# Kernel optimization log

Measured on AMD Instinct MI355X. Metric: run time of the kernel, lower is better.

The kernel has to match this reference:

```python
import jax, jax.numpy as jnp
import numpy as np

N, C_IN, C_OUT, W_DIM, H, W = 16, 512, 512, 512, 64, 64

def setup_inputs() -> dict:
    key = jax.random.key(0)
    ks = jax.random.split(key, 6)
    return {
        "x": jax.random.normal(ks[0], (N, C_IN, H, W), dtype=jnp.float32),
        "w": jax.random.normal(ks[1], (N, W_DIM), dtype=jnp.float32),
        "noise": jax.random.normal(ks[2], (N, 1, H, W), dtype=jnp.float32),
        "affine_w": jax.random.normal(ks[3], (C_IN, W_DIM), dtype=jnp.float32) * (1.0 / np.sqrt(W_DIM)),
        "affine_b": jnp.ones((C_IN,), dtype=jnp.float32),  # bias_init=1.0
        "noise_strength": jnp.ones((), dtype=jnp.float32),
        "conv_w": jax.random.normal(ks[4], (C_OUT, C_IN, 3, 3), dtype=jnp.float32),
        "conv_b": jnp.zeros((C_OUT,), dtype=jnp.float32),
    }

def reference(x, w, noise, affine_w, affine_b, noise_strength, conv_w, conv_b):
    # affine: s = w @ affine_w.T + affine_b  (no activation)
    s = jnp.einsum('nd,cd->nc', w, affine_w) + affine_b  # [N, C_in]
    # Demodulated per-sample conv. Original builds w_n = W * s_n then demodulates;
    # since conv is linear in the weight's input-channel scale, this is equivalent to
    # scaling the input by s and the output by the demod factor d.
    w2 = jnp.sum(conv_w * conv_w, axis=(2, 3))  # [O, I]: sum over kernel taps
    d = jax.lax.rsqrt(jnp.einsum('ni,oi->no', s * s, w2) + 1e-8)  # [N, O]
    x_mod = x * s[:, :, None, None]
    y = jax.lax.conv_general_dilated(
        x_mod, conv_w, window_strides=(1, 1), padding='SAME',
        dimension_numbers=('NCHW', 'OIHW', 'NCHW'))  # [N, O, H, W]
    y = y * d[:, :, None, None] + conv_b[None, :, None, None]
    y = y + noise * noise_strength
    return jnp.where(y >= 0, y, 0.2 * y)  # LeakyReLU(0.2)
```

## Files before the change

kernel.cpp:

```cpp
#include <hip/hip_runtime.h>
#include <hip/hip_bf16.h>

typedef unsigned short u16;
typedef short bf16x8 __attribute__((ext_vector_type(8)));
typedef float f32x4 __attribute__((ext_vector_type(4)));

#define N_    16
#define CIN   512
#define COUT  512
#define WD    512
#define P_    4096
#define CC    (COUT * CIN)

#define OFF_S   0u
#define OFF_D   32768u
#define OFF_Z   65536u
#define OFF_WBT 131072u
#define OFF_XB  8388608u
#define WS_NEED (OFF_XB + 67108864u)

__device__ __forceinline__ u16 f2bf(float f) {
  union { float f; unsigned u; } a; a.f = f;
  unsigned r = a.u + 0x7fffu + ((a.u >> 16) & 1u);
  return (u16)(r >> 16);
}

__device__ __forceinline__ void gl_lds16(const u16* g, u16* l) {
  __builtin_amdgcn_global_load_lds(
      (const __attribute__((address_space(1))) void*)g,
      (__attribute__((address_space(3))) void*)l, 16, 0, 0);
}

__global__ void k_zero(float* z) { z[threadIdx.x] = 0.f; }

__global__ __launch_bounds__(256) void k_affine(const float* __restrict__ w,
                                                const float* __restrict__ aw,
                                                const float* __restrict__ ab,
                                                float* __restrict__ s) {
  int idx = blockIdx.x * 256 + threadIdx.x;
  int n = idx >> 9, c = idx & 511;
  const float4* wr = (const float4*)(w + (size_t)n * WD);
  const float4* ar = (const float4*)(aw + (size_t)c * WD);
  float acc = 0.f;
#pragma unroll 4
  for (int k = 0; k < WD / 4; ++k) {
    float4 a = wr[k], b = ar[k];
    acc += a.x * b.x + a.y * b.y + a.z * b.z + a.w * b.w;
  }
  s[idx] = acc + ab[c];
}

__global__ __launch_bounds__(256) void k_demod(const float* __restrict__ s,
                                               const float* __restrict__ cw,
                                               float* __restrict__ d) {
  __shared__ float w2[CIN];
  int o = blockIdx.x;
  const float* wr = cw + (size_t)o * CIN * 9;
  for (int i = threadIdx.x; i < CIN; i += 256) {
    float acc = 0.f;
#pragma unroll
    for (int t = 0; t < 9; ++t) { float v = wr[i * 9 + t]; acc += v * v; }
    w2[i] = acc;
  }
  __syncthreads();
  int wave = threadIdx.x >> 6, lane = threadIdx.x & 63;
  for (int nn = wave; nn < N_; nn += 4) {
    float acc = 0.f;
    for (int i = lane; i < CIN; i += 64) {
      float sv = s[nn * CIN + i];
      acc += sv * sv * w2[i];
    }
#pragma unroll
    for (int off = 32; off > 0; off >>= 1) acc += __shfl_down(acc, off);
    if (lane == 0) {
      float a = acc + 1e-8f;
      float r = rsqrtf(a);
      r = r * (1.5f - 0.5f * a * r * r);
      d[nn * COUT + o] = r;
    }
  }
}

__global__ __launch_bounds__(256) void k_wprep(const float* __restrict__ cw,
                                               u16* __restrict__ wbt) {
  int idx = blockIdx.x * 256 + threadIdx.x;
  if (idx >= COUT * CIN * 9) return;
  int t = idx % 9; int oi = idx / 9; int i = oi & 511; int o = oi >> 9;
  wbt[((size_t)t * COUT + o) * CIN + i] = f2bf(cw[idx]);
}

__global__ __launch_bounds__(256) void k_xmod(const float* __restrict__ x,
                                              const float* __restrict__ s,
                                              u16* __restrict__ xb) {
  __shared__ float tile[64][65];
  int b = blockIdx.x;
  int pt = b & 63; int ct = (b >> 6) & 7; int n = b >> 9;
  int c0 = ct * 64, p0 = pt * 64;
  const float* xp = x + ((size_t)n * CIN + c0) * P_ + p0;
  int t = threadIdx.x;
#pragma unroll
  for (int pass = 0; pass < 4; ++pass) {
    int r = pass * 16 + (t >> 4);
    int col4 = (t & 15);
    float4 v = *(const float4*)(xp + (size_t)r * P_ + col4 * 4);
    float sc = s[n * CIN + c0 + r];
    tile[r][col4 * 4 + 0] = v.x * sc;
    tile[r][col4 * 4 + 1] = v.y * sc;
    tile[r][col4 * 4 + 2] = v.z * sc;
    tile[r][col4 * 4 + 3] = v.w * sc;
  }
  __syncthreads();
  int p = t >> 2, cq = (t & 3) * 16;
  union { u16 us[16]; uint4 q[2]; } pk;
#pragma unroll
  for (int j = 0; j < 16; ++j) pk.us[j] = f2bf(tile[cq + j][p]);
  uint4* dst = (uint4*)(xb + ((size_t)n * P_ + p0 + p) * CIN + c0 + cq);
  dst[0] = pk.q[0];
  dst[1] = pk.q[1];
}

__global__ __launch_bounds__(512, 2) void k_conv(const u16* __restrict__ xb,
                                                 const u16* __restrict__ wbt,
                                                 const u16* __restrict__ zp,
                                                 const float* __restrict__ dmod,
                                                 const float* __restrict__ cbias,
                                                 const float* __restrict__ noise,
                                                 const float* __restrict__ nstr,
                                                 float* __restrict__ out) {
  __shared__ u16 smA[4][8192];
  __shared__ u16 smB[4][8192];

  int bid = blockIdx.x;
  int wg = (bid & 7) * 64 + (bid >> 3);
  int n = wg >> 5;
  int rem = wg & 31;
  int ob = rem >> 4;
  int pb = rem & 15;

  int tid = threadIdx.x;
  int wv = tid >> 6, l = tid & 63;
  int wr = wv >> 2, wc = wv & 3;
  int lrow = l & 15, kgrp = l >> 4;
  int prs = kgrp ^ ((lrow >> 1) & 3);

  int srow = tid >> 2;
  int lslot = (tid & 3) ^ ((tid >> 3) & 3);
  const u16* xbn = xb + (size_t)n * P_ * CIN;
  int hg[2], wgp[2];
#pragma unroll
  for (int g = 0; g < 2; ++g) {
    int ploc = g * 128 + srow;
    hg[g] = pb * 4 + (ploc >> 6);
    wgp[g] = ploc & 63;
  }
  const u16* srcA_base[2];
#pragma unroll
  for (int g = 0; g < 2; ++g)
    srcA_base[g] = wbt + (size_t)(ob * 256 + g * 128 + srow) * CIN + lslot * 8;

  auto stage_A = [&](int tt) {
    int b = tt & 3;
    int tapn = tt >> 4, cbn = tt & 15;
#pragma unroll
    for (int g = 0; g < 2; ++g) {
      const u16* src = srcA_base[g] + (size_t)tapn * CC + cbn * 32;
      gl_lds16(src, &smA[b][g * 4096 + wv * 512]);
    }
  };
  auto bsrc_for_tap = [&](int tapn, int g) -> const u16* {
    int dh = tapn < 3 ? -1 : (tapn < 6 ? 0 : 1);
    int dw = tapn - (dh + 1) * 3 - 1;
    int hh = hg[g] + dh, ww = wgp[g] + dw;
    bool val = ((unsigned)hh < 64u) && ((unsigned)ww < 64u);
    return val ? (xbn + ((size_t)((hh << 6) + ww)) * CIN + lslot * 8)
               : (zp + lslot * 8);
  };
  auto stage_B = [&](int tt) {
    int b = tt & 3;
    int tapn = tt >> 4, cbn = tt & 15;
#pragma unroll
    for (int g = 0; g < 2; ++g)
      gl_lds16(bsrc_for_tap(tapn, g) + cbn * 32, &smB[b][g * 4096 + wv * 512]);
  };

  f32x4 acc0[4][4], acc1[4][4];
  f32x4 zero = {0.f, 0.f, 0.f, 0.f};
#pragma unroll
  for (int i = 0; i < 4; ++i)
#pragma unroll
    for (int j = 0; j < 4; ++j) { acc0[i][j] = zero; acc1[i][j] = zero; }

  stage_A(0); stage_B(0);
  stage_A(1); stage_B(1);
  stage_A(2); stage_B(2);

  int tap3 = 0, cb3 = 3;
  const u16* rpA[2];
  const u16* rpB[2];
#pragma unroll
  for (int g = 0; g < 2; ++g) {
    rpA[g] = srcA_base[g] + 3 * 32;
    rpB[g] = bsrc_for_tap(0, g) + 3 * 32;
  }

  for (int t = 0; t < 144; ++t) {
    int b = t & 3;
    int bs = (t + 3) & 3;
    if (t <= 141)      asm volatile("s_waitcnt vmcnt(8)" ::: "memory");
    else if (t == 142) asm volatile("s_waitcnt vmcnt(4)" ::: "memory");
    else               asm volatile("s_waitcnt vmcnt(0)" ::: "memory");
    __builtin_amdgcn_s_barrier();
    __builtin_amdgcn_sched_barrier(0);

    const u16* A = smA[b];
    const u16* B = smB[b];

    bf16x8 Bf[4], Af0[4], Af1[4];
#pragma unroll
    for (int mi = 0; mi < 4; ++mi)
      Af0[mi] = *(const bf16x8*)&A[(wr * 128 + mi * 16 + lrow) * 32 + prs * 8];
    __builtin_amdgcn_sched_barrier(0);
#pragma unroll
    for (int ni = 0; ni < 4; ++ni)
      Bf[ni] = *(const bf16x8*)&B[(wc * 64 + ni * 16 + lrow) * 32 + prs * 8];
    __builtin_amdgcn_sched_barrier(0);
#pragma unroll
    for (int mi = 0; mi < 4; ++mi)
      Af1[mi] = *(const bf16x8*)&A[(wr * 128 + 64 + mi * 16 + lrow) * 32 + prs * 8];
    __builtin_amdgcn_sched_barrier(0);

    if (t <= 140) {
#pragma unroll
      for (int g = 0; g < 2; ++g)
        gl_lds16(rpA[g], &smA[bs][g * 4096 + wv * 512]);
#pragma unroll
      for (int g = 0; g < 2; ++g)
        gl_lds16(rpB[g], &smB[bs][g * 4096 + wv * 512]);
      cb3++;
      if (cb3 == 16) {
        cb3 = 0; tap3++;
#pragma unroll
        for (int g = 0; g < 2; ++g) {
          rpA[g] = srcA_base[g] + (size_t)tap3 * CC;
          rpB[g] = bsrc_for_tap(tap3, g);
        }
      } else {
#pragma unroll
        for (int g = 0; g < 2; ++g) { rpA[g] += 32; rpB[g] += 32; }
      }
    }
    __builtin_amdgcn_sched_barrier(0);

    __builtin_amdgcn_s_setprio(1);
#pragma unroll
    for (int ni = 0; ni < 4; ++ni) {
      if (ni == 0)      asm volatile("s_waitcnt lgkmcnt(7)" ::: "memory");
      else if (ni == 1) asm volatile("s_waitcnt lgkmcnt(6)" ::: "memory");
      else if (ni == 2) asm volatile("s_waitcnt lgkmcnt(5)" ::: "memory");
      else              asm volatile("s_waitcnt lgkmcnt(4)" ::: "memory");
      __builtin_amdgcn_sched_barrier(0);
#pragma unroll
      for (int mi = 0; mi < 4; ++mi)
        acc0[mi][ni] = __builtin_amdgcn_mfma_f32_16x16x32_bf16(
            Af0[mi], Bf[ni], acc0[mi][ni], 0, 0, 0);
    }

    asm volatile("s_waitcnt lgkmcnt(0)" ::: "memory");
    __builtin_amdgcn_sched_barrier(0);
#pragma unroll
    for (int mi = 0; mi < 4; ++mi)
#pragma unroll
      for (int ni = 0; ni < 4; ++ni)
        acc1[mi][ni] = __builtin_amdgcn_mfma_f32_16x16x32_bf16(
            Af1[mi], Bf[ni], acc1[mi][ni], 0, 0, 0);
    __builtin_amdgcn_s_setprio(0);
  }

  float ns = nstr[0];
  const float* noise_n = noise + (size_t)n * P_;
  float nz[4];
#pragma unroll
  for (int ni = 0; ni < 4; ++ni)
    nz[ni] = noise_n[pb * 256 + wc * 64 + ni * 16 + lrow] * ns;

  auto epi = [&](f32x4 (&A_)[4][4], int qm) {
#pragma unroll
    for (int mi = 0; mi < 4; ++mi) {
      int o0 = ob * 256 + wr * 128 + qm * 64 + mi * 16 + kgrp * 4;
#pragma unroll
      for (int r = 0; r < 4; ++r) {
        int o = o0 + r;
        float dv = dmod[n * COUT + o];
        float bv = cbias[o];
        float* orow = out + ((size_t)(n * COUT + o)) * P_ + pb * 256 + wc * 64;
#pragma unroll
        for (int ni = 0; ni < 4; ++ni) {
          float v = A_[mi][ni][r] * dv + bv + nz[ni];
          orow[ni * 16 + lrow] = v >= 0.f ? v : 0.2f * v;
        }
      }
    }
  };
  epi(acc0, 0);
  epi(acc1, 1);
}

__global__ __launch_bounds__(64) void k_conv_naive(const float* __restrict__ x,
                                                   const float* __restrict__ cw,
                                                   const float* __restrict__ cbias,
                                                   const float* __restrict__ noise,
                                                   const float* __restrict__ nstr,
                                                   const float* __restrict__ s,
                                                   const float* __restrict__ d,
                                                   float* __restrict__ out) {
  int bid = blockIdx.x;
  int h = bid & 63; int o = (bid >> 6) & 511; int n = bid >> 15;
  int wcol = threadIdx.x;
  float acc = 0.f;
  for (int i = 0; i < CIN; ++i) {
    float sv = s[n * CIN + i];
    const float* xrow = x + ((size_t)(n * CIN + i)) * P_;
    const float* wrp = cw + ((size_t)o * CIN + i) * 9;
#pragma unroll
    for (int t = 0; t < 9; ++t) {
      int hh = h + t / 3 - 1, ww = wcol + t % 3 - 1;
      float xv = ((unsigned)hh < 64u && (unsigned)ww < 64u) ? xrow[hh * 64 + ww] : 0.f;
      acc += xv * sv * wrp[t];
    }
  }
  float v = acc * d[n * COUT + o] + cbias[o] + noise[(size_t)n * P_ + h * 64 + wcol] * nstr[0];
  out[((size_t)(n * COUT + o)) * P_ + h * 64 + wcol] = v >= 0.f ? v : 0.2f * v;
}

extern "C" void kernel_launch(void* const* d_in, const int* in_sizes, int n_in,
                              void* d_out, int out_size, void* d_ws, size_t ws_size,
                              hipStream_t stream) {
  const float* x    = (const float*)d_in[0];
  const float* w    = (const float*)d_in[1];
  const float* noise= (const float*)d_in[2];
  const float* aw   = (const float*)d_in[3];
  const float* ab   = (const float*)d_in[4];
  const float* nstr = (const float*)d_in[5];
  const float* cw   = (const float*)d_in[6];
  const float* cb   = (const float*)d_in[7];
  float* out = (float*)d_out;
  char* ws = (char*)d_ws;
  float* s = (float*)(ws + OFF_S);
  float* d = (float*)(ws + OFF_D);

  k_affine<<<(N_ * COUT) / 256, 256, 0, stream>>>(w, aw, ab, s);
  k_demod<<<COUT, 256, 0, stream>>>(s, cw, d);

  if (ws_size >= WS_NEED) {
    u16* zp  = (u16*)(ws + OFF_Z);
    u16* wbt = (u16*)(ws + OFF_WBT);
    u16* xbb = (u16*)(ws + OFF_XB);
    k_zero<<<1, 256, 0, stream>>>((float*)zp);
    k_wprep<<<(COUT * CIN * 9 + 255) / 256, 256, 0, stream>>>(cw, wbt);
    k_xmod<<<N_ * 8 * 64, 256, 0, stream>>>(x, s, xbb);
    k_conv<<<512, 512, 0, stream>>>(xbb, wbt, zp, d, cb, noise, nstr, out);
  } else {
    k_conv_naive<<<N_ * COUT * 64, 64, 0, stream>>>(x, cw, cb, noise, nstr, s, d, out);
  }
}
```

Baseline: 339.3 us.

## Process two K-tiles per barrier in the implicit-GEMM conv main loop

Restructures the 144-step main loop into 72 iterations that each consume two LDS stages under a single barrier, with a vmcnt(0) wait instead of vmcnt(8). The prefetch distance drops from three tiles to two, and two stage_next calls are interleaved between the MFMA groups. The goal is to halve barrier count and interleave LDS reads with MFMA work. The risk is exposed global-load latency from the full vmcnt(0) drain and the shallower prefetch, plus higher register pressure from holding fragments for two tiles.

```diff
diff --git a/kernel.cpp b/kernel.cpp
--- a/kernel.cpp
+++ b/kernel.cpp
@@ -158,15 +158,6 @@
   for (int g = 0; g < 2; ++g)
     srcA_base[g] = wbt + (size_t)(ob * 256 + g * 128 + srow) * CIN + lslot * 8;
 
-  auto stage_A = [&](int tt) {
-    int b = tt & 3;
-    int tapn = tt >> 4, cbn = tt & 15;
-#pragma unroll
-    for (int g = 0; g < 2; ++g) {
-      const u16* src = srcA_base[g] + (size_t)tapn * CC + cbn * 32;
-      gl_lds16(src, &smA[b][g * 4096 + wv * 512]);
-    }
-  };
   auto bsrc_for_tap = [&](int tapn, int g) -> const u16* {
     int dh = tapn < 3 ? -1 : (tapn < 6 ? 0 : 1);
     int dw = tapn - (dh + 1) * 3 - 1;
@@ -175,9 +166,14 @@
     return val ? (xbn + ((size_t)((hh << 6) + ww)) * CIN + lslot * 8)
                : (zp + lslot * 8);
   };
-  auto stage_B = [&](int tt) {
+  auto stage_tile = [&](int tt) {
     int b = tt & 3;
     int tapn = tt >> 4, cbn = tt & 15;
+#pragma unroll
+    for (int g = 0; g < 2; ++g) {
+      const u16* src = srcA_base[g] + (size_t)tapn * CC + cbn * 32;
+      gl_lds16(src, &smA[b][g * 4096 + wv * 512]);
+    }
 #pragma unroll
     for (int g = 0; g < 2; ++g)
       gl_lds16(bsrc_for_tap(tapn, g) + cbn * 32, &smB[b][g * 4096 + wv * 512]);
@@ -190,65 +186,67 @@
 #pragma unroll
     for (int j = 0; j < 4; ++j) { acc0[i][j] = zero; acc1[i][j] = zero; }
 
-  stage_A(0); stage_B(0);
-  stage_A(1); stage_B(1);
-  stage_A(2); stage_B(2);
-
-  int tap3 = 0, cb3 = 3;
+  stage_tile(0);
+  stage_tile(1);
+
+  int ts = 2, tap3 = 0, cb3 = 2;
   const u16* rpA[2];
   const u16* rpB[2];
 #pragma unroll
   for (int g = 0; g < 2; ++g) {
-    rpA[g] = srcA_base[g] + 3 * 32;
-    rpB[g] = bsrc_for_tap(0, g) + 3 * 32;
-  }
-
-  for (int t = 0; t < 144; ++t) {
-    int b = t & 3;
-    int bs = (t + 3) & 3;
-    if (t <= 141)      asm volatile("s_waitcnt vmcnt(8)" ::: "memory");
-    else if (t == 142) asm volatile("s_waitcnt vmcnt(4)" ::: "memory");
-    else               asm volatile("s_waitcnt vmcnt(0)" ::: "memory");
+    rpA[g] = srcA_base[g] + 2 * 32;
+    rpB[g] = bsrc_for_tap(0, g) + 2 * 32;
+  }
+  auto stage_next = [&]() {
+    int bs = ts & 3;
+#pragma unroll
+    for (int g = 0; g < 2; ++g)
+      gl_lds16(rpA[g], &smA[bs][g * 4096 + wv * 512]);
+#pragma unroll
+    for (int g = 0; g < 2; ++g)
+      gl_lds16(rpB[g], &smB[bs][g * 4096 + wv * 512]);
+    ++ts;
+    cb3++;
+    if (cb3 == 16) {
+      cb3 = 0; tap3++;
+#pragma unroll
+      for (int g = 0; g < 2; ++g) {
+        rpA[g] = srcA_base[g] + (size_t)tap3 * CC;
+        rpB[g] = bsrc_for_tap(tap3, g);
+      }
+    } else {
+#pragma unroll
+      for (int g = 0; g < 2; ++g) { rpA[g] += 32; rpB[g] += 32; }
+    }
+  };
+
+  for (int k = 0; k < 72; ++k) {
+    int a = 2 * k;
+    const u16* A0 = smA[a & 3];
+    const u16* B0 = smB[a & 3];
+    const u16* A1 = smA[(a + 1) & 3];
+    const u16* B1 = smB[(a + 1) & 3];
+
+    asm volatile("s_waitcnt vmcnt(0)" ::: "memory");
     __builtin_amdgcn_s_barrier();
     __builtin_amdgcn_sched_barrier(0);
 
-    const u16* A = smA[b];
-    const u16* B = smB[b];
-
-    bf16x8 Bf[4], Af0[4], Af1[4];
-#pragma unroll
-    for (int mi = 0; mi < 4; ++mi)
-      Af0[mi] = *(const bf16x8*)&A[(wr * 128 + mi * 16 + lrow) * 32 + prs * 8];
+    bf16x8 Af0a[4], Bfa[4], Af1a[4], Af0b[4], Bfb[4], Af1b[4];
+
+#pragma unroll
+    for (int mi = 0; mi < 4; ++mi)
+      Af0a[mi] = *(const bf16x8*)&A0[(wr * 128 + mi * 16 + lrow) * 32 + prs * 8];
     __builtin_amdgcn_sched_barrier(0);
 #pragma unroll
     for (int ni = 0; ni < 4; ++ni)
-      Bf[ni] = *(const bf16x8*)&B[(wc * 64 + ni * 16 + lrow) * 32 + prs * 8];
-    __builtin_amdgcn_sched_barrier(0);
-#pragma unroll
-    for (int mi = 0; mi < 4; ++mi)
-      Af1[mi] = *(const bf16x8*)&A[(wr * 128 + 64 + mi * 16 + lrow) * 32 + prs * 8];
-    __builtin_amdgcn_sched_barrier(0);
-
-    if (t <= 140) {
-#pragma unroll
-      for (int g = 0; g < 2; ++g)
-        gl_lds16(rpA[g], &smA[bs][g * 4096 + wv * 512]);
-#pragma unroll
-      for (int g = 0; g < 2; ++g)
-        gl_lds16(rpB[g], &smB[bs][g * 4096 + wv * 512]);
-      cb3++;
-      if (cb3 == 16) {
-        cb3 = 0; tap3++;
-#pragma unroll
-        for (int g = 0; g < 2; ++g) {
-          rpA[g] = srcA_base[g] + (size_t)tap3 * CC;
-          rpB[g] = bsrc_for_tap(tap3, g);
-        }
-      } else {
-#pragma unroll
-        for (int g = 0; g < 2; ++g) { rpA[g] += 32; rpB[g] += 32; }
-      }
-    }
+      Bfa[ni] = *(const bf16x8*)&B0[(wc * 64 + ni * 16 + lrow) * 32 + prs * 8];
+    __builtin_amdgcn_sched_barrier(0);
+#pragma unroll
+    for (int mi = 0; mi < 4; ++mi)
+      Af1a[mi] = *(const bf16x8*)&A0[(wr * 128 + 64 + mi * 16 + lrow) * 32 + prs * 8];
+    __builtin_amdgcn_sched_barrier(0);
+
+    if (k <= 70) stage_next();
     __builtin_amdgcn_sched_barrier(0);
 
     __builtin_amdgcn_s_setprio(1);
@@ -262,17 +260,61 @@
 #pragma unroll
       for (int mi = 0; mi < 4; ++mi)
         acc0[mi][ni] = __builtin_amdgcn_mfma_f32_16x16x32_bf16(
-            Af0[mi], Bf[ni], acc0[mi][ni], 0, 0, 0);
-    }
-
-    asm volatile("s_waitcnt lgkmcnt(0)" ::: "memory");
+            Af0a[mi], Bfa[ni], acc0[mi][ni], 0, 0, 0);
+    }
+    __builtin_amdgcn_s_setprio(0);
+    __builtin_amdgcn_sched_barrier(0);
+
+#pragma unroll
+    for (int mi = 0; mi < 4; ++mi)
+      Af0b[mi] = *(const bf16x8*)&A1[(wr * 128 + mi * 16 + lrow) * 32 + prs * 8];
+    __builtin_amdgcn_sched_barrier(0);
+#pragma unroll
+    for (int ni = 0; ni < 4; ++ni)
+      Bfb[ni] = *(const bf16x8*)&B1[(wc * 64 + ni * 16 + lrow) * 32 + prs * 8];
+    __builtin_amdgcn_sched_barrier(0);
+
+    __builtin_amdgcn_s_setprio(1);
+    asm volatile("s_waitcnt lgkmcnt(8)" ::: "memory");
     __builtin_amdgcn_sched_barrier(0);
 #pragma unroll
     for (int mi = 0; mi < 4; ++mi)
 #pragma unroll
       for (int ni = 0; ni < 4; ++ni)
         acc1[mi][ni] = __builtin_amdgcn_mfma_f32_16x16x32_bf16(
-            Af1[mi], Bf[ni], acc1[mi][ni], 0, 0, 0);
+            Af1a[mi], Bfa[ni], acc1[mi][ni], 0, 0, 0);
+    __builtin_amdgcn_s_setprio(0);
+    __builtin_amdgcn_sched_barrier(0);
+
+#pragma unroll
+    for (int mi = 0; mi < 4; ++mi)
+      Af1b[mi] = *(const bf16x8*)&A1[(wr * 128 + 64 + mi * 16 + lrow) * 32 + prs * 8];
+    __builtin_amdgcn_sched_barrier(0);
+    if (k <= 70) stage_next();
+    __builtin_amdgcn_sched_barrier(0);
+
+    __builtin_amdgcn_s_setprio(1);
+#pragma unroll
+    for (int ni = 0; ni < 4; ++ni) {
+      if (ni == 0)      asm volatile("s_waitcnt lgkmcnt(7)" ::: "memory");
+      else if (ni == 1) asm volatile("s_waitcnt lgkmcnt(6)" ::: "memory");
+      else if (ni == 2) asm volatile("s_waitcnt lgkmcnt(5)" ::: "memory");
+      else              asm volatile("s_waitcnt lgkmcnt(4)" ::: "memory");
+      __builtin_amdgcn_sched_barrier(0);
+#pragma unroll
+      for (int mi = 0; mi < 4; ++mi)
+        acc0[mi][ni] = __builtin_amdgcn_mfma_f32_16x16x32_bf16(
+            Af0b[mi], Bfb[ni], acc0[mi][ni], 0, 0, 0);
+    }
+
+    asm volatile("s_waitcnt lgkmcnt(0)" ::: "memory");
+    __builtin_amdgcn_sched_barrier(0);
+#pragma unroll
+    for (int mi = 0; mi < 4; ++mi)
+#pragma unroll
+      for (int ni = 0; ni < 4; ++ni)
+        acc1[mi][ni] = __builtin_amdgcn_mfma_f32_16x16x32_bf16(
+            Af1b[mi], Bfb[ni], acc1[mi][ni], 0, 0, 0);
     __builtin_amdgcn_s_setprio(0);
   }
 
```

After: 336.9 us. Within noise of the previous version (-0.7%).
